# Kernel tuning notes

Measured on AMD Instinct MI355X. Metric: run time of the kernel, lower is better.

The kernel has to match this reference:

```python
import jax, jax.numpy as jnp
import numpy as np

B, S, H = 128, 1024, 768
MAX_VERBS = 25
S_LEVI = S - 2 * MAX_VERBS  # start of levitated marker block (single_marker=False)


def setup_inputs() -> dict:
    key = jax.random.key(0)
    k = jax.random.split(key, 6)
    return {
        "hidden": jax.random.normal(k[0], (B, S, H), dtype=jnp.float32),
        "verb_count": jax.random.randint(k[1], (B,), 0, 25, dtype=jnp.int64),
        "subject_hidden": jax.random.normal(k[2], (B, H), dtype=jnp.float32),
        "align_w": jax.random.normal(k[3], (1, 2 * H), dtype=jnp.float32) * 0.02,
        "align_b": jnp.zeros((1,), dtype=jnp.float32),
        "out_w": jax.random.normal(k[4], (H, H), dtype=jnp.float32) * 0.02,
        "out_b": jnp.zeros((H,), dtype=jnp.float32),
    }


def _token_mask(verb_count):
    # pair-marker mask: [s_levi, s_levi+v) U [s_levi+MAX_VERBS, s_levi+MAX_VERBS+v)
    w_ids = jnp.arange(S)[None, :]            # [1, S]
    v = verb_count[:, None]                   # [B, 1]
    m_start = (w_ids >= S_LEVI) & (w_ids < S_LEVI + v)
    m_end = (w_ids >= S_LEVI + MAX_VERBS) & (w_ids < S_LEVI + MAX_VERBS + v)
    return m_start | m_end                    # [B, S] bool


def reference(hidden, verb_count, subject_hidden, align_w, align_b, out_w, out_b):
    mask = _token_mask(verb_count)                       # [B, S]
    maskf = mask[..., None]
    masked = jnp.where(maskf, hidden, 0.0)               # [B, S, H]
    subj = jnp.where(maskf, subject_hidden[:, None, :], 0.0)  # [B, S, H]
    # alignment_model(cat([subj, masked], -1)) -> [B, S] scores
    scores = (jnp.einsum("bsh,h->bs", subj, align_w[0, :H])
              + jnp.einsum("bsh,h->bs", masked, align_w[0, H:])
              + align_b[0])
    # per-example masked softmax over the selected (marker) positions
    m = jnp.max(jnp.where(mask, scores, -jnp.inf), axis=1, keepdims=True)
    m = jnp.where(jnp.isfinite(m), m, 0.0)               # guard all-masked rows
    e = jnp.where(mask, jnp.exp(scores - m), 0.0)
    denom = jnp.sum(e, axis=1, keepdims=True)
    weights = jnp.where(denom > 0, e / jnp.maximum(denom, 1e-30), 0.0)  # [B, S]
    pooled = jnp.einsum("bs,bsh->bh", weights, masked)   # [B, H]
    # output_layer: Linear + Tanh
    return jnp.tanh(pooled @ out_w.T + out_b)
```

## Files before the change

kernel.cpp:

```cpp
#include <hip/hip_runtime.h>
#include <math.h>

#define BSZ   128
#define SSZ   1024
#define HSZ   768
#define MAXV  25
#define SLEVI (SSZ - 2 * MAXV)

__global__ __launch_bounds__(256) void pool_kernel(
    const float* __restrict__ hidden,
    const int*   __restrict__ verb_count,
    const float* __restrict__ align_w,
    float*       __restrict__ pooled)
{
    const int b    = blockIdx.x;
    const int tid  = threadIdx.x;
    const int lane = tid & 63;
    const int wave = tid >> 6;

    int v = verb_count[b];
    if (v < 0)    v = 0;
    if (v > MAXV) v = MAXV;
    const int nt = 2 * v;

    __shared__ float sc [2 * MAXV];
    __shared__ float wts[2 * MAXV];

    const float* __restrict__ w2 = align_w + HSZ;

    for (int t = wave; t < nt; t += 4) {
        const int s = (t < v) ? (SLEVI + t) : (SLEVI + MAXV + (t - v));
        const float* __restrict__ row = hidden + ((size_t)b * SSZ + s) * HSZ;
        float acc = 0.0f;
#pragma unroll
        for (int i = 0; i < HSZ / 64; ++i) {
            acc = fmaf(row[lane + 64 * i], w2[lane + 64 * i], acc);
        }
#pragma unroll
        for (int off = 32; off > 0; off >>= 1) {
            acc += __shfl_down(acc, off);
        }
        if (lane == 0) sc[t] = acc;
    }
    __syncthreads();

    if (tid == 0 && nt > 0) {
        float m = -INFINITY;
        for (int t = 0; t < nt; ++t) m = fmaxf(m, sc[t]);
        float denom = 0.0f;
        for (int t = 0; t < nt; ++t) {
            const float e = expf(sc[t] - m);
            wts[t] = e;
            denom += e;
        }
        const float inv = 1.0f / denom;
        for (int t = 0; t < nt; ++t) wts[t] *= inv;
    }
    __syncthreads();

    float acc0 = 0.0f, acc1 = 0.0f, acc2 = 0.0f;
    for (int t = 0; t < nt; ++t) {
        const int s = (t < v) ? (SLEVI + t) : (SLEVI + MAXV + (t - v));
        const float w = wts[t];
        const float* __restrict__ row = hidden + ((size_t)b * SSZ + s) * HSZ;
        acc0 = fmaf(w, row[tid          ], acc0);
        acc1 = fmaf(w, row[tid + 256    ], acc1);
        acc2 = fmaf(w, row[tid + 512    ], acc2);
    }
    float* dst = pooled + (size_t)b * HSZ;
    dst[tid      ] = acc0;
    dst[tid + 256] = acc1;
    dst[tid + 512] = acc2;
}

#define BPB 4

__global__ __launch_bounds__(256) void gemv_tanh_kernel(
    const float* __restrict__ pooled,
    const float* __restrict__ out_w,
    const float* __restrict__ out_b,
    float*       __restrict__ out)
{
    const int i  = blockIdx.x * 256 + threadIdx.x;
    const int b0 = blockIdx.y * BPB;

    const float* __restrict__ wrow = out_w + (size_t)i * HSZ;

    float acc[BPB];
#pragma unroll
    for (int bb = 0; bb < BPB; ++bb) acc[bb] = 0.0f;

    for (int j = 0; j < HSZ; j += 4) {
        const float4 w4 = *(const float4*)(wrow + j);
#pragma unroll
        for (int bb = 0; bb < BPB; ++bb) {
            const float4 p4 = *(const float4*)(pooled + (size_t)(b0 + bb) * HSZ + j);
            acc[bb] = fmaf(w4.x, p4.x, acc[bb]);
            acc[bb] = fmaf(w4.y, p4.y, acc[bb]);
            acc[bb] = fmaf(w4.z, p4.z, acc[bb]);
            acc[bb] = fmaf(w4.w, p4.w, acc[bb]);
        }
    }

    const float bias = out_b[i];
#pragma unroll
    for (int bb = 0; bb < BPB; ++bb) {
        out[(size_t)(b0 + bb) * HSZ + i] = tanhf(acc[bb] + bias);
    }
}

extern "C" void kernel_launch(void* const* d_in, const int* in_sizes, int n_in,
                              void* d_out, int out_size, void* d_ws, size_t ws_size,
                              hipStream_t stream) {
    const float* hidden     = (const float*)d_in[0];
    const int*   verb_count = (const int*)  d_in[1];
    const float* align_w    = (const float*)d_in[3];
    const float* out_w      = (const float*)d_in[5];
    const float* out_b      = (const float*)d_in[6];
    float*       out        = (float*)d_out;
    float*       pooled     = (float*)d_ws;

    pool_kernel<<<dim3(BSZ), dim3(256), 0, stream>>>(hidden, verb_count, align_w, pooled);

    gemv_tanh_kernel<<<dim3(HSZ / 256, BSZ / BPB), dim3(256), 0, stream>>>(
        pooled, out_w, out_b, out);
}
```

Baseline: 486.5 us.

## Fuse pooling and output GEMV+tanh into one per-batch kernel

Merges the pooling kernel and the output linear+tanh kernel into a single kernel with one block per batch row, keeping the pooled vector in shared memory instead of writing it to workspace. The softmax becomes a wave-wide shuffle reduction instead of a serial single-thread loop, and the score and pooling loads use float4. The cost is that each of the 128 blocks now reads the whole 768x768 out_w matrix with row-strided per-thread float4 loads. That means more total weight traffic (mostly L2-served) and only 128 blocks of parallelism for the GEMV.

```diff
diff --git a/kernel.cpp b/kernel.cpp
--- a/kernel.cpp
+++ b/kernel.cpp
@@ -7,11 +7,13 @@
 #define MAXV  25
 #define SLEVI (SSZ - 2 * MAXV)
 
-__global__ __launch_bounds__(256) void pool_kernel(
+__global__ __launch_bounds__(256) void fused_pooler_kernel(
     const float* __restrict__ hidden,
     const int*   __restrict__ verb_count,
     const float* __restrict__ align_w,
-    float*       __restrict__ pooled)
+    const float* __restrict__ out_w,
+    const float* __restrict__ out_b,
+    float*       __restrict__ out)
 {
     const int b    = blockIdx.x;
     const int tid  = threadIdx.x;
@@ -23,8 +25,9 @@
     if (v > MAXV) v = MAXV;
     const int nt = 2 * v;
 
-    __shared__ float sc [2 * MAXV];
-    __shared__ float wts[2 * MAXV];
+    __shared__ float sc    [2 * MAXV];
+    __shared__ float wts   [2 * MAXV];
+    __shared__ float pooled[HSZ];
 
     const float* __restrict__ w2 = align_w + HSZ;
 
@@ -33,79 +36,72 @@
         const float* __restrict__ row = hidden + ((size_t)b * SSZ + s) * HSZ;
         float acc = 0.0f;
 #pragma unroll
-        for (int i = 0; i < HSZ / 64; ++i) {
-            acc = fmaf(row[lane + 64 * i], w2[lane + 64 * i], acc);
+        for (int k = 0; k < 3; ++k) {
+            const int idx = 4 * lane + 256 * k;
+            const float4 r = *(const float4*)(row + idx);
+            const float4 w = *(const float4*)(w2  + idx);
+            acc = fmaf(r.x, w.x, acc);
+            acc = fmaf(r.y, w.y, acc);
+            acc = fmaf(r.z, w.z, acc);
+            acc = fmaf(r.w, w.w, acc);
         }
 #pragma unroll
-        for (int off = 32; off > 0; off >>= 1) {
-            acc += __shfl_down(acc, off);
-        }
+        for (int off = 32; off > 0; off >>= 1) acc += __shfl_down(acc, off);
         if (lane == 0) sc[t] = acc;
     }
     __syncthreads();
 
-    if (tid == 0 && nt > 0) {
-        float m = -INFINITY;
-        for (int t = 0; t < nt; ++t) m = fmaxf(m, sc[t]);
-        float denom = 0.0f;
-        for (int t = 0; t < nt; ++t) {
-            const float e = expf(sc[t] - m);
-            wts[t] = e;
-            denom += e;
-        }
-        const float inv = 1.0f / denom;
-        for (int t = 0; t < nt; ++t) wts[t] *= inv;
+    if (wave == 0) {
+        float x = (lane < nt) ? sc[lane] : -INFINITY;
+        float m = x;
+#pragma unroll
+        for (int off = 32; off > 0; off >>= 1) m = fmaxf(m, __shfl_xor(m, off));
+        const float e = (lane < nt) ? expf(x - m) : 0.0f;
+        float d = e;
+#pragma unroll
+        for (int off = 32; off > 0; off >>= 1) d += __shfl_xor(d, off);
+        if (lane < nt) wts[lane] = e / d;
     }
     __syncthreads();
 
-    float acc0 = 0.0f, acc1 = 0.0f, acc2 = 0.0f;
-    for (int t = 0; t < nt; ++t) {
-        const int s = (t < v) ? (SLEVI + t) : (SLEVI + MAXV + (t - v));
-        const float w = wts[t];
-        const float* __restrict__ row = hidden + ((size_t)b * SSZ + s) * HSZ;
-        acc0 = fmaf(w, row[tid          ], acc0);
-        acc1 = fmaf(w, row[tid + 256    ], acc1);
-        acc2 = fmaf(w, row[tid + 512    ], acc2);
+    if (tid < HSZ / 4) {
+        float4 acc = make_float4(0.f, 0.f, 0.f, 0.f);
+        const float* __restrict__ base = hidden + ((size_t)b * SSZ) * HSZ + 4 * tid;
+        for (int t = 0; t < nt; ++t) {
+            const int s = (t < v) ? (SLEVI + t) : (SLEVI + MAXV + (t - v));
+            const float w = wts[t];
+            const float4 r = *(const float4*)(base + (size_t)s * HSZ);
+            acc.x = fmaf(w, r.x, acc.x);
+            acc.y = fmaf(w, r.y, acc.y);
+            acc.z = fmaf(w, r.z, acc.z);
+            acc.w = fmaf(w, r.w, acc.w);
+        }
+        *(float4*)(pooled + 4 * tid) = acc;
     }
-    float* dst = pooled + (size_t)b * HSZ;
-    dst[tid      ] = acc0;
-    dst[tid + 256] = acc1;
-    dst[tid + 512] = acc2;
-}
+    __syncthreads();
 
-#define BPB 4
-
-__global__ __launch_bounds__(256) void gemv_tanh_kernel(
-    const float* __restrict__ pooled,
-    const float* __restrict__ out_w,
-    const float* __restrict__ out_b,
-    float*       __restrict__ out)
-{
-    const int i  = blockIdx.x * 256 + threadIdx.x;
-    const int b0 = blockIdx.y * BPB;
-
-    const float* __restrict__ wrow = out_w + (size_t)i * HSZ;
-
-    float acc[BPB];
-#pragma unroll
-    for (int bb = 0; bb < BPB; ++bb) acc[bb] = 0.0f;
-
-    for (int j = 0; j < HSZ; j += 4) {
-        const float4 w4 = *(const float4*)(wrow + j);
-#pragma unroll
-        for (int bb = 0; bb < BPB; ++bb) {
-            const float4 p4 = *(const float4*)(pooled + (size_t)(b0 + bb) * HSZ + j);
-            acc[bb] = fmaf(w4.x, p4.x, acc[bb]);
-            acc[bb] = fmaf(w4.y, p4.y, acc[bb]);
-            acc[bb] = fmaf(w4.z, p4.z, acc[bb]);
-            acc[bb] = fmaf(w4.w, p4.w, acc[bb]);
+    {
+        const float* __restrict__ wr0 = out_w + (size_t)(tid      ) * HSZ;
+        const float* __restrict__ wr1 = out_w + (size_t)(tid + 256) * HSZ;
+        const float* __restrict__ wr2 = out_w + (size_t)(tid + 512) * HSZ;
+        float a0 = 0.f, a1 = 0.f, a2 = 0.f;
+#pragma unroll 4
+        for (int j = 0; j < HSZ; j += 4) {
+            const float4 p  = *(const float4*)(pooled + j);
+            const float4 x0 = *(const float4*)(wr0 + j);
+            const float4 x1 = *(const float4*)(wr1 + j);
+            const float4 x2 = *(const float4*)(wr2 + j);
+            a0 = fmaf(x0.x, p.x, a0); a0 = fmaf(x0.y, p.y, a0);
+            a0 = fmaf(x0.z, p.z, a0); a0 = fmaf(x0.w, p.w, a0);
+            a1 = fmaf(x1.x, p.x, a1); a1 = fmaf(x1.y, p.y, a1);
+            a1 = fmaf(x1.z, p.z, a1); a1 = fmaf(x1.w, p.w, a1);
+            a2 = fmaf(x2.x, p.x, a2); a2 = fmaf(x2.y, p.y, a2);
+            a2 = fmaf(x2.z, p.z, a2); a2 = fmaf(x2.w, p.w, a2);
         }
-    }
-
-    const float bias = out_b[i];
-#pragma unroll
-    for (int bb = 0; bb < BPB; ++bb) {
-        out[(size_t)(b0 + bb) * HSZ + i] = tanhf(acc[bb] + bias);
+        float* __restrict__ dst = out + (size_t)b * HSZ;
+        dst[tid      ] = tanhf(a0 + out_b[tid      ]);
+        dst[tid + 256] = tanhf(a1 + out_b[tid + 256]);
+        dst[tid + 512] = tanhf(a2 + out_b[tid + 512]);
     }
 }
 
@@ -118,10 +114,7 @@
     const float* out_w      = (const float*)d_in[5];
     const float* out_b      = (const float*)d_in[6];
     float*       out        = (float*)d_out;
-    float*       pooled     = (float*)d_ws;
 
-    pool_kernel<<<dim3(BSZ), dim3(256), 0, stream>>>(hidden, verb_count, align_w, pooled);
-
-    gemv_tanh_kernel<<<dim3(HSZ / 256, BSZ / BPB), dim3(256), 0, stream>>>(
-        pooled, out_w, out_b, out);
+    fused_pooler_kernel<<<dim3(BSZ), dim3(256), 0, stream>>>(
+        hidden, verb_count, align_w, out_w, out_b, out);
 }
```

Result: slower. 511.3 us (+5.1%).
